# Kernel optimization log

Measured on AMD Instinct MI355X. Metric: run time of the kernel, lower is better.

Reference implementation:

```python
import jax, jax.numpy as jnp
import numpy as np

B, S, E, H = 2, 2048, 1024, 16
DH = E // H  # 64


def setup_inputs() -> dict:
    key = jax.random.key(0)
    ks = jax.random.split(key, 5)
    scale = 1.0 / np.sqrt(E)
    x = jax.random.normal(ks[0], (B, S, E), dtype=jnp.float32)
    # stacked per-head kqv Linear weights: out = x @ Wkqv[h] + bkqv[h], producing (k, q, v) chunks
    Wkqv = jax.random.normal(ks[1], (H, E, 3 * DH), dtype=jnp.float32) * scale
    bkqv = jax.random.normal(ks[2], (H, 3 * DH), dtype=jnp.float32) * scale
    Wo = jax.random.normal(ks[3], (E, E), dtype=jnp.float32) * scale
    bo = jax.random.normal(ks[4], (E,), dtype=jnp.float32) * scale
    return {"x": x, "Wkqv": Wkqv, "bkqv": bkqv, "Wo": Wo, "bo": bo}


def reference(x, Wkqv, bkqv, Wo, bo):
    b, s, e = x.shape
    h, _, f = Wkqv.shape
    dh = f // 3
    # per-head projection, fused over heads: [b, h, s, 3*dh]
    kqv = jnp.einsum('bse,hef->bhsf', x, Wkqv) + bkqv[None, :, None, :]
    # chunk order in the original is k, q, v
    k, q, v = jnp.split(kqv, 3, axis=-1)
    scores = jnp.einsum('bhqd,bhkd->bhqk', q, k) / jnp.sqrt(jnp.asarray(dh, x.dtype))
    causal = jnp.tril(jnp.ones((s, s), dtype=bool))  # slice of the tril buffer
    scores = jnp.where(causal[None, None], scores, -jnp.inf)
    weights = jax.nn.softmax(scores, axis=-1)
    sa = jnp.einsum('bhqk,bhkd->bhqd', weights, v)
    # concat heads along feature dim (head order preserved)
    sa = sa.transpose(0, 2, 1, 3).reshape(b, s, h * dh)
    return sa @ Wo + bo
```

## Files before the change

### kernel.cpp

```cpp
#include <hip/hip_runtime.h>
#include <hip/hip_bf16.h>

typedef __attribute__((ext_vector_type(8))) short bf16x8;
typedef __attribute__((ext_vector_type(4))) float f32x4;
typedef unsigned short u16;

#define NEG_INF (-__builtin_inff())

__device__ __forceinline__ void gload16(const void* g, void* l) {
  __builtin_amdgcn_global_load_lds(
      (const __attribute__((address_space(1))) void*)g,
      (__attribute__((address_space(3))) void*)l, 16, 0, 0);
}

__device__ __forceinline__ u16 f2b(float f) {
  union { float f; unsigned u; } v;
  v.f = f;
  unsigned r = v.u + 0x7fff + ((v.u >> 16) & 1);
  return (u16)(r >> 16);
}

__global__ __launch_bounds__(256) void cvt_f2b_kernel(
    const float* __restrict__ in, u16* __restrict__ out, int n4) {
  int i = blockIdx.x * 256 + threadIdx.x;
  if (i >= n4) return;
  float4 v = ((const float4*)in)[i];
  ushort2 a = {f2b(v.x), f2b(v.y)}, b = {f2b(v.z), f2b(v.w)};
  ((ushort2*)out)[i * 2] = a;
  ((ushort2*)out)[i * 2 + 1] = b;
}

__global__ __launch_bounds__(256) void transpose_f2b(
    const float* __restrict__ src, u16* __restrict__ dst, int R, int C) {
  __shared__ u16 t[32][33];
  int c0 = blockIdx.x * 32, r0 = blockIdx.y * 32;
  const float* s = src + (size_t)blockIdx.z * R * C;
  u16* d = dst + (size_t)blockIdx.z * R * C;
  for (int i = threadIdx.y; i < 32; i += 8)
    t[i][threadIdx.x] = f2b(s[(size_t)(r0 + i) * C + c0 + threadIdx.x]);
  __syncthreads();
  for (int i = threadIdx.y; i < 32; i += 8)
    d[(size_t)(c0 + i) * R + r0 + threadIdx.x] = t[threadIdx.x][i];
}

__device__ __forceinline__ void gemm_mainloop_128(
    const __hip_bfloat16* __restrict__ A, const __hip_bfloat16* __restrict__ Bt,
    int K, int m0, int n0, f32x4 acc[4][4], char* AsB, char* BsB) {
  const int tid = threadIdx.x;
  const int wave = tid >> 6, lane = tid & 63;
  const int lhi = lane >> 4, llo = lane & 15;
  const int wr = wave >> 1, wc = wave & 1;
  f32x4 z = {0.f, 0.f, 0.f, 0.f};
#pragma unroll
  for (int i = 0; i < 4; i++)
#pragma unroll
    for (int j = 0; j < 4; j++) acc[i][j] = z;

#define GSTAGE(c, kk)                                                          \
  {                                                                            \
    char* AsW = AsB + (c)*8192;                                                \
    char* BsW = BsB + (c)*8192;                                                \
    _Pragma("unroll") for (int i = 0; i < 2; i++) {                            \
      int cb = i * 256 + wave * 64;                                            \
      int cq = cb + lane;                                                      \
      gload16(A + ((size_t)(m0 + (cq >> 2)) * K + (kk) + (cq & 3) * 8),        \
              AsW + cb * 16);                                                  \
      gload16(Bt + ((size_t)(n0 + (cq >> 2)) * K + (kk) + (cq & 3) * 8),       \
              BsW + cb * 16);                                                  \
    }                                                                          \
  }

  GSTAGE(0, 0);
  int cur = 0;
  const int nk = K >> 5;
  for (int t = 0; t < nk; t++) {
    if (t + 1 < nk) {
      GSTAGE(cur ^ 1, (t + 1) * 32);
      asm volatile("s_waitcnt vmcnt(4)" ::: "memory");
    } else {
      asm volatile("s_waitcnt vmcnt(0)" ::: "memory");
    }
    __builtin_amdgcn_s_barrier();
    __builtin_amdgcn_sched_barrier(0);

    const char* Ar = AsB + cur * 8192;
    const char* Br = BsB + cur * 8192;
    bf16x8 a[4], b[4];
#pragma unroll
    for (int m4 = 0; m4 < 4; m4++)
      a[m4] = *(const bf16x8*)(Ar + (wr * 64 + m4 * 16 + llo) * 64 + lhi * 16);
#pragma unroll
    for (int n4 = 0; n4 < 4; n4++)
      b[n4] = *(const bf16x8*)(Br + (wc * 64 + n4 * 16 + llo) * 64 + lhi * 16);
#pragma unroll
    for (int m4 = 0; m4 < 4; m4++)
#pragma unroll
      for (int n4 = 0; n4 < 4; n4++)
        acc[m4][n4] =
            __builtin_amdgcn_mfma_f32_16x16x32_bf16(a[m4], b[n4], acc[m4][n4], 0, 0, 0);
    __builtin_amdgcn_sched_barrier(0);
    __builtin_amdgcn_s_barrier();
    cur ^= 1;
  }
#undef GSTAGE
}

__global__ __launch_bounds__(256) void kqv_gemm(
    const __hip_bfloat16* __restrict__ x, const __hip_bfloat16* __restrict__ WT,
    const float* __restrict__ bkqv, __hip_bfloat16* __restrict__ Qb,
    __hip_bfloat16* __restrict__ Kb, __hip_bfloat16* __restrict__ Vt) {
  __shared__ __align__(16) char As[16384];
  __shared__ __align__(16) char Bs[16384];
  const int m0 = blockIdx.y * 128, n0 = blockIdx.x * 128;
  f32x4 acc[4][4];
  gemm_mainloop_128(x, WT, 1024, m0, n0, acc, As, Bs);

  const int tid = threadIdx.x, wave = tid >> 6, lane = tid & 63;
  const int lhi = lane >> 4, llo = lane & 15;
  const int wr = wave >> 1, wc = wave & 1;
#pragma unroll
  for (int m4 = 0; m4 < 4; m4++)
#pragma unroll
    for (int n4 = 0; n4 < 4; n4++)
#pragma unroll
      for (int r = 0; r < 4; r++) {
        int mg = m0 + wr * 64 + m4 * 16 + lhi * 4 + r;
        int ng = n0 + wc * 64 + n4 * 16 + llo;
        int b = mg >> 11, s = mg & 2047;
        int h = ng / 192, f = ng % 192;
        float v = acc[m4][n4][r] + bkqv[h * 192 + f];
        int chunk = f >> 6, d = f & 63;
        size_t bh = (size_t)(b * 16 + h);
        if (chunk == 0)
          Kb[(bh * 2048 + s) * 64 + d] = __float2bfloat16(v);
        else if (chunk == 1)
          Qb[(bh * 2048 + s) * 64 + d] = __float2bfloat16(v * 0.180336880f);
        else
          Vt[(bh * 64 + d) * 2048 + s] = __float2bfloat16(v);
      }
}

__global__ __launch_bounds__(256) void attn_kernel(
    const __hip_bfloat16* __restrict__ Qb, const __hip_bfloat16* __restrict__ Kb,
    const __hip_bfloat16* __restrict__ Vt, __hip_bfloat16* __restrict__ SA) {
  __shared__ __align__(16) char lds[40960];
  const int bx0 = blockIdx.x;
  const int bx = (bx0 & 7) * 64 + (bx0 >> 3);
  const int bh = bx >> 4;
  const int ip = bx & 15;
  const int qa = 31 - ip, qbt = ip;
  const int nta = qa + 1, nt = nta + qbt + 1;
  const int b = bh >> 4, h = bh & 15;
  const int tid = threadIdx.x, wave = tid >> 6, lane = tid & 63;
  const int lhi = lane >> 4, llo = lane & 15;
  const int lhi4 = lhi * 4;

  const __hip_bfloat16* qpA =
      Qb + ((size_t)bh * 2048 + qa * 64 + wave * 16 + llo) * 64 + lhi * 8;
  const __hip_bfloat16* qpB =
      Qb + ((size_t)bh * 2048 + qbt * 64 + wave * 16 + llo) * 64 + lhi * 8;
  bf16x8 qA0 = *(const bf16x8*)qpA, qA1 = *(const bf16x8*)(qpA + 32);
  bf16x8 qB0 = *(const bf16x8*)qpB, qB1 = *(const bf16x8*)(qpB + 32);
  bf16x8 q0 = qA0, q1 = qA1;

  const char* Kg = (const char*)(Kb + (size_t)bh * 2048 * 64);
  const char* Vg = (const char*)(Vt + (size_t)bh * 64 * 2048);
  char* PsB = lds + 32768 + wave * 2048;

  f32x4 z = {0.f, 0.f, 0.f, 0.f};
  f32x4 o[4];
  float m_s = NEG_INF, l_s = 0.f;
#pragma unroll
  for (int i = 0; i < 4; i++) o[i] = z;
  int qg = qa * 64 + wave * 16 + llo;
  int qg0 = qa * 64 + wave * 16 + lhi4;

#define STAGE(c, k0)                                                          \
  {                                                                           \
    char* KsW = lds + (c)*8192;                                               \
    char* VsW = lds + 16384 + (c)*8192;                                       \
    _Pragma("unroll") for (int i = 0; i < 2; i++) {                           \
      int ch = i * 256 + tid;                                                 \
      int soff = (ch * 16) ^ (((ch >> 3) & 7) << 4);                          \
      gload16(Kg + (size_t)(k0)*128 + soff, KsW + (i * 256 + wave * 64) * 16);\
      int dd = ch >> 3, c8 = ch & 7;                                          \
      int boff = (c8 * 16) ^ ((dd & 7) << 4);                                 \
      gload16(Vg + (size_t)dd * 4096 + (size_t)(k0)*2 + boff,                 \
              VsW + (i * 256 + wave * 64) * 16);                              \
    }                                                                         \
  }

  STAGE(0, 0);
  int cur = 0;

  for (int T = 0; T < nt; T++) {
    const int Tn = T + 1;
    if (Tn < nt) {
      const int k0n = (Tn < nta ? Tn : Tn - nta) * 64;
      STAGE(cur ^ 1, k0n);
      asm volatile("s_waitcnt vmcnt(4)" ::: "memory");
    } else {
      asm volatile("s_waitcnt vmcnt(0)" ::: "memory");
    }
    __builtin_amdgcn_s_barrier();
    __builtin_amdgcn_sched_barrier(0);

    const int k0 = (T < nta ? T : T - nta) * 64;
    const bool masked = (T == nta - 1) || (T == nt - 1);
    const char* KsB = lds + cur * 8192;
    const char* VsB = lds + 16384 + cur * 8192;

    f32x4 s[4] = {z, z, z, z};
#pragma unroll
    for (int j = 0; j < 4; j++) {
      const int row = j * 16 + llo;
      const int rx = (row & 7) << 4;
      bf16x8 bk0 = *(const bf16x8*)(KsB + ((row * 128 + lhi * 16) ^ rx));
      bf16x8 bk1 = *(const bf16x8*)(KsB + ((row * 128 + 64 + lhi * 16) ^ rx));
      s[j] = __builtin_amdgcn_mfma_f32_16x16x32_bf16(bk0, q0, s[j], 0, 0, 0);
      s[j] = __builtin_amdgcn_mfma_f32_16x16x32_bf16(bk1, q1, s[j], 0, 0, 0);
    }

    if (masked) {
#pragma unroll
      for (int j = 0; j < 4; j++)
#pragma unroll
        for (int r = 0; r < 4; r++)
          if (k0 + j * 16 + lhi4 + r > qg) s[j][r] = NEG_INF;
    }
    float pmax = s[0][0];
#pragma unroll
    for (int j = 0; j < 4; j++)
#pragma unroll
      for (int r = 0; r < 4; r++) pmax = fmaxf(pmax, s[j][r]);
    pmax = fmaxf(pmax, __shfl_xor(pmax, 16));
    pmax = fmaxf(pmax, __shfl_xor(pmax, 32));
    if (!__all(pmax - m_s <= 5.0f)) {
      const float mn = fmaxf(m_s, pmax);
      const float sc = __builtin_exp2f(m_s - mn);
      m_s = mn;
      l_s *= sc;
#pragma unroll
      for (int r = 0; r < 4; r++) {
        const float scr = __shfl(sc, lhi4 + r);
#pragma unroll
        for (int n4 = 0; n4 < 4; n4++) o[n4][r] *= scr;
      }
    }
    const int px = (llo & 7) << 4;
    float ps = 0.f;
#pragma unroll
    for (int j = 0; j < 4; j++) {
      ushort4 pw;
#pragma unroll
      for (int r = 0; r < 4; r++) {
        const float p = __builtin_exp2f(s[j][r] - m_s);
        ps += p;
        ((__hip_bfloat16*)&pw)[r] = __float2bfloat16(p);
      }
      *(ushort4*)(PsB + ((llo * 128 + j * 32 + lhi * 8) ^ px)) = pw;
    }
    l_s += ps;

    {
      bf16x8 ap0 = *(const bf16x8*)(PsB + ((llo * 128 + lhi * 16) ^ px));
      bf16x8 ap1 = *(const bf16x8*)(PsB + ((llo * 128 + 64 + lhi * 16) ^ px));
#pragma unroll
      for (int n4 = 0; n4 < 4; n4++) {
        const int d = n4 * 16 + llo;
        const int dx = (d & 7) << 4;
        bf16x8 bv0 = *(const bf16x8*)(VsB + ((d * 128 + lhi * 16) ^ dx));
        bf16x8 bv1 = *(const bf16x8*)(VsB + ((d * 128 + 64 + lhi * 16) ^ dx));
        o[n4] = __builtin_amdgcn_mfma_f32_16x16x32_bf16(ap0, bv0, o[n4], 0, 0, 0);
        o[n4] = __builtin_amdgcn_mfma_f32_16x16x32_bf16(ap1, bv1, o[n4], 0, 0, 0);
      }
    }
    __builtin_amdgcn_sched_barrier(0);
    __builtin_amdgcn_s_barrier();

    if (T == nta - 1) {
      float l = l_s;
      l += __shfl_xor(l, 16);
      l += __shfl_xor(l, 32);
      const float inv = 1.f / l;
#pragma unroll
      for (int r = 0; r < 4; r++) {
        const float invr = __shfl(inv, lhi4 + r);
        const size_t ob = ((size_t)b * 2048 + qg0 + r) * 1024 + h * 64;
#pragma unroll
        for (int n4 = 0; n4 < 4; n4++)
          SA[ob + n4 * 16 + llo] = __float2bfloat16(o[n4][r] * invr);
      }
#pragma unroll
      for (int i = 0; i < 4; i++) o[i] = z;
      m_s = NEG_INF;
      l_s = 0.f;
      q0 = qB0; q1 = qB1;
      qg = qbt * 64 + wave * 16 + llo;
      qg0 = qbt * 64 + wave * 16 + lhi4;
    }
    cur ^= 1;
  }

  {
    float l = l_s;
    l += __shfl_xor(l, 16);
    l += __shfl_xor(l, 32);
    const float inv = 1.f / l;
#pragma unroll
    for (int r = 0; r < 4; r++) {
      const float invr = __shfl(inv, lhi4 + r);
      const size_t ob = ((size_t)b * 2048 + qg0 + r) * 1024 + h * 64;
#pragma unroll
      for (int n4 = 0; n4 < 4; n4++)
        SA[ob + n4 * 16 + llo] = __float2bfloat16(o[n4][r] * invr);
    }
  }
#undef STAGE
}

__global__ __launch_bounds__(256) void out_gemm(
    const __hip_bfloat16* __restrict__ SA, const __hip_bfloat16* __restrict__ WoT,
    const float* __restrict__ bo, float* __restrict__ out) {
  __shared__ __align__(16) char As[16384];
  __shared__ __align__(16) char Bs[16384];
  const int m0 = blockIdx.y * 128, n0 = blockIdx.x * 128;
  f32x4 acc[4][4];
  gemm_mainloop_128(SA, WoT, 1024, m0, n0, acc, As, Bs);

  const int tid = threadIdx.x, wave = tid >> 6, lane = tid & 63;
  const int lhi = lane >> 4, llo = lane & 15;
  const int wr = wave >> 1, wc = wave & 1;
#pragma unroll
  for (int m4 = 0; m4 < 4; m4++)
#pragma unroll
    for (int n4 = 0; n4 < 4; n4++)
#pragma unroll
      for (int r = 0; r < 4; r++) {
        int mg = m0 + wr * 64 + m4 * 16 + lhi * 4 + r;
        int ng = n0 + wc * 64 + n4 * 16 + llo;
        out[(size_t)mg * 1024 + ng] = acc[m4][n4][r] + bo[ng];
      }
}

extern "C" void kernel_launch(void* const* d_in, const int* in_sizes, int n_in,
                              void* d_out, int out_size, void* d_ws, size_t ws_size,
                              hipStream_t stream) {
  const float* x = (const float*)d_in[0];
  const float* Wkqv = (const float*)d_in[1];
  const float* bkqv = (const float*)d_in[2];
  const float* Wo = (const float*)d_in[3];
  const float* bo = (const float*)d_in[4];
  float* out = (float*)d_out;

  char* w = (char*)d_ws;
  __hip_bfloat16* WkqvT = (__hip_bfloat16*)(w);
  __hip_bfloat16* WoT = (__hip_bfloat16*)(w + 6291456);
  __hip_bfloat16* Qb = (__hip_bfloat16*)(w + 8388608);
  __hip_bfloat16* Kb = (__hip_bfloat16*)(w + 16777216);
  __hip_bfloat16* Vt = (__hip_bfloat16*)(w + 25165824);
  __hip_bfloat16* SAb = (__hip_bfloat16*)(w + 33554432);
  __hip_bfloat16* xb = (__hip_bfloat16*)(w + 41943040);

  cvt_f2b_kernel<<<4096, 256, 0, stream>>>(x, (u16*)xb, 1048576);
  transpose_f2b<<<dim3(6, 32, 16), dim3(32, 8, 1), 0, stream>>>(
      Wkqv, (u16*)WkqvT, 1024, 192);
  transpose_f2b<<<dim3(32, 32, 1), dim3(32, 8, 1), 0, stream>>>(
      Wo, (u16*)WoT, 1024, 1024);
  kqv_gemm<<<dim3(24, 32), 256, 0, stream>>>(xb, WkqvT, bkqv, Qb, Kb, Vt);
  attn_kernel<<<512, 256, 0, stream>>>(Qb, Kb, Vt, SAb);
  out_gemm<<<dim3(8, 32), 256, 0, stream>>>(SAb, WoT, bo, out);
}
```

Measured before the change: 130.2 us.

## Fuse prep kernels, split attention into one q-tile per block, shrink out GEMM tile

Merges the three conversion/transpose kernels into one prep launch to cut launch overhead. Attention switches from paired heavy/light q-tiles per block to one q-tile per block, launched heaviest first, doubling the grid to 1024 blocks. The output GEMM moves to a 64x128 tile with 512 blocks to fill more CUs. The trade is more blocks with less work each, and tile-level load balance now depends on the hardware scheduler rather than explicit pairing.

```diff
diff --git a/kernel.cpp b/kernel.cpp
--- a/kernel.cpp
+++ b/kernel.cpp
@@ -20,27 +20,42 @@
   return (u16)(r >> 16);
 }
 
-__global__ __launch_bounds__(256) void cvt_f2b_kernel(
-    const float* __restrict__ in, u16* __restrict__ out, int n4) {
-  int i = blockIdx.x * 256 + threadIdx.x;
-  if (i >= n4) return;
-  float4 v = ((const float4*)in)[i];
-  ushort2 a = {f2b(v.x), f2b(v.y)}, b = {f2b(v.z), f2b(v.w)};
-  ((ushort2*)out)[i * 2] = a;
-  ((ushort2*)out)[i * 2 + 1] = b;
-}
-
-__global__ __launch_bounds__(256) void transpose_f2b(
-    const float* __restrict__ src, u16* __restrict__ dst, int R, int C) {
+__global__ __launch_bounds__(256) void prep_kernel(
+    const float* __restrict__ x, u16* __restrict__ xb,
+    const float* __restrict__ Wkqv, u16* __restrict__ WkqvT,
+    const float* __restrict__ Wo, u16* __restrict__ WoT) {
   __shared__ u16 t[32][33];
-  int c0 = blockIdx.x * 32, r0 = blockIdx.y * 32;
-  const float* s = src + (size_t)blockIdx.z * R * C;
-  u16* d = dst + (size_t)blockIdx.z * R * C;
-  for (int i = threadIdx.y; i < 32; i += 8)
-    t[i][threadIdx.x] = f2b(s[(size_t)(r0 + i) * C + c0 + threadIdx.x]);
+  const int bid = blockIdx.x;
+  const int tid = threadIdx.x;
+  if (bid < 4096) {
+    const int i = bid * 256 + tid;
+    float4 v = ((const float4*)x)[i];
+    ushort2 a = {f2b(v.x), f2b(v.y)}, b = {f2b(v.z), f2b(v.w)};
+    ((ushort2*)xb)[i * 2] = a;
+    ((ushort2*)xb)[i * 2 + 1] = b;
+    return;
+  }
+  const int tx = tid & 31, ty = tid >> 5;
+  const float* src;
+  u16* dst;
+  int R, C, bx_, by;
+  if (bid < 7168) {
+    const int tt = bid - 4096;
+    const int bz = tt / 192, rem = tt % 192;
+    by = rem / 6; bx_ = rem % 6; R = 1024; C = 192;
+    src = Wkqv + (size_t)bz * R * C;
+    dst = WkqvT + (size_t)bz * R * C;
+  } else {
+    const int tt = bid - 7168;
+    by = tt >> 5; bx_ = tt & 31; R = 1024; C = 1024;
+    src = Wo; dst = WoT;
+  }
+  const int c0 = bx_ * 32, r0 = by * 32;
+  for (int i = ty; i < 32; i += 8)
+    t[i][tx] = f2b(src[(size_t)(r0 + i) * C + c0 + tx]);
   __syncthreads();
-  for (int i = threadIdx.y; i < 32; i += 8)
-    d[(size_t)(c0 + i) * R + r0 + threadIdx.x] = t[threadIdx.x][i];
+  for (int i = ty; i < 32; i += 8)
+    dst[(size_t)(c0 + i) * R + r0 + tx] = t[tx][i];
 }
 
 __device__ __forceinline__ void gemm_mainloop_128(
@@ -103,6 +118,68 @@
     cur ^= 1;
   }
 #undef GSTAGE
+}
+
+__device__ __forceinline__ void gemm_mainloop_64x128(
+    const __hip_bfloat16* __restrict__ A, const __hip_bfloat16* __restrict__ Bt,
+    int K, int m0, int n0, f32x4 acc[2][4], char* AsB, char* BsB) {
+  const int tid = threadIdx.x;
+  const int wave = tid >> 6, lane = tid & 63;
+  const int lhi = lane >> 4, llo = lane & 15;
+  const int wr = wave >> 1, wc = wave & 1;
+  f32x4 z = {0.f, 0.f, 0.f, 0.f};
+#pragma unroll
+  for (int i = 0; i < 2; i++)
+#pragma unroll
+    for (int j = 0; j < 4; j++) acc[i][j] = z;
+
+#define GSTAGE64(c, kk)                                                        \
+  {                                                                            \
+    char* AsW = AsB + (c)*4096;                                                \
+    char* BsW = BsB + (c)*8192;                                                \
+    gload16(A + ((size_t)(m0 + (tid >> 2)) * K + (kk) + (tid & 3) * 8),        \
+            AsW + (wave * 64) * 16);                                           \
+    _Pragma("unroll") for (int i = 0; i < 2; i++) {                            \
+      int cb = i * 256 + wave * 64;                                            \
+      int cq = cb + lane;                                                      \
+      gload16(Bt + ((size_t)(n0 + (cq >> 2)) * K + (kk) + (cq & 3) * 8),       \
+              BsW + cb * 16);                                                  \
+    }                                                                          \
+  }
+
+  GSTAGE64(0, 0);
+  int cur = 0;
+  const int nk = K >> 5;
+  for (int t = 0; t < nk; t++) {
+    if (t + 1 < nk) {
+      GSTAGE64(cur ^ 1, (t + 1) * 32);
+      asm volatile("s_waitcnt vmcnt(3)" ::: "memory");
+    } else {
+      asm volatile("s_waitcnt vmcnt(0)" ::: "memory");
+    }
+    __builtin_amdgcn_s_barrier();
+    __builtin_amdgcn_sched_barrier(0);
+
+    const char* Ar = AsB + cur * 4096;
+    const char* Br = BsB + cur * 8192;
+    bf16x8 a[2], b[4];
+#pragma unroll
+    for (int m2 = 0; m2 < 2; m2++)
+      a[m2] = *(const bf16x8*)(Ar + (wr * 32 + m2 * 16 + llo) * 64 + lhi * 16);
+#pragma unroll
+    for (int n4 = 0; n4 < 4; n4++)
+      b[n4] = *(const bf16x8*)(Br + (wc * 64 + n4 * 16 + llo) * 64 + lhi * 16);
+#pragma unroll
+    for (int m2 = 0; m2 < 2; m2++)
+#pragma unroll
+      for (int n4 = 0; n4 < 4; n4++)
+        acc[m2][n4] =
+            __builtin_amdgcn_mfma_f32_16x16x32_bf16(a[m2], b[n4], acc[m2][n4], 0, 0, 0);
+    __builtin_amdgcn_sched_barrier(0);
+    __builtin_amdgcn_s_barrier();
+    cur ^= 1;
+  }
+#undef GSTAGE64
 }
 
 __global__ __launch_bounds__(256) void kqv_gemm(
@@ -144,24 +221,18 @@
     const __hip_bfloat16* __restrict__ Qb, const __hip_bfloat16* __restrict__ Kb,
     const __hip_bfloat16* __restrict__ Vt, __hip_bfloat16* __restrict__ SA) {
   __shared__ __align__(16) char lds[40960];
-  const int bx0 = blockIdx.x;
-  const int bx = (bx0 & 7) * 64 + (bx0 >> 3);
-  const int bh = bx >> 4;
-  const int ip = bx & 15;
-  const int qa = 31 - ip, qbt = ip;
-  const int nta = qa + 1, nt = nta + qbt + 1;
+  const int orig = blockIdx.x;
+  const int bh = (orig & 7) * 4 + ((orig >> 3) & 3);
+  const int qt = 31 - (orig >> 5);
+  const int nt = qt + 1;
   const int b = bh >> 4, h = bh & 15;
   const int tid = threadIdx.x, wave = tid >> 6, lane = tid & 63;
   const int lhi = lane >> 4, llo = lane & 15;
   const int lhi4 = lhi * 4;
 
-  const __hip_bfloat16* qpA =
-      Qb + ((size_t)bh * 2048 + qa * 64 + wave * 16 + llo) * 64 + lhi * 8;
-  const __hip_bfloat16* qpB =
-      Qb + ((size_t)bh * 2048 + qbt * 64 + wave * 16 + llo) * 64 + lhi * 8;
-  bf16x8 qA0 = *(const bf16x8*)qpA, qA1 = *(const bf16x8*)(qpA + 32);
-  bf16x8 qB0 = *(const bf16x8*)qpB, qB1 = *(const bf16x8*)(qpB + 32);
-  bf16x8 q0 = qA0, q1 = qA1;
+  const __hip_bfloat16* qp =
+      Qb + ((size_t)bh * 2048 + qt * 64 + wave * 16 + llo) * 64 + lhi * 8;
+  bf16x8 q0 = *(const bf16x8*)qp, q1 = *(const bf16x8*)(qp + 32);
 
   const char* Kg = (const char*)(Kb + (size_t)bh * 2048 * 64);
   const char* Vg = (const char*)(Vt + (size_t)bh * 64 * 2048);
@@ -172,8 +243,8 @@
   float m_s = NEG_INF, l_s = 0.f;
 #pragma unroll
   for (int i = 0; i < 4; i++) o[i] = z;
-  int qg = qa * 64 + wave * 16 + llo;
-  int qg0 = qa * 64 + wave * 16 + lhi4;
+  const int qg = qt * 64 + wave * 16 + llo;
+  const int qg0 = qt * 64 + wave * 16 + lhi4;
 
 #define STAGE(c, k0)                                                          \
   {                                                                           \
@@ -194,10 +265,8 @@
   int cur = 0;
 
   for (int T = 0; T < nt; T++) {
-    const int Tn = T + 1;
-    if (Tn < nt) {
-      const int k0n = (Tn < nta ? Tn : Tn - nta) * 64;
-      STAGE(cur ^ 1, k0n);
+    if (T + 1 < nt) {
+      STAGE(cur ^ 1, (T + 1) * 64);
       asm volatile("s_waitcnt vmcnt(4)" ::: "memory");
     } else {
       asm volatile("s_waitcnt vmcnt(0)" ::: "memory");
@@ -205,8 +274,8 @@
     __builtin_amdgcn_s_barrier();
     __builtin_amdgcn_sched_barrier(0);
 
-    const int k0 = (T < nta ? T : T - nta) * 64;
-    const bool masked = (T == nta - 1) || (T == nt - 1);
+    const int k0 = T * 64;
+    const bool masked = (T == nt - 1);
     const char* KsB = lds + cur * 8192;
     const char* VsB = lds + 16384 + cur * 8192;
 
@@ -277,28 +346,6 @@
     }
     __builtin_amdgcn_sched_barrier(0);
     __builtin_amdgcn_s_barrier();
-
-    if (T == nta - 1) {
-      float l = l_s;
-      l += __shfl_xor(l, 16);
-      l += __shfl_xor(l, 32);
-      const float inv = 1.f / l;
-#pragma unroll
-      for (int r = 0; r < 4; r++) {
-        const float invr = __shfl(inv, lhi4 + r);
-        const size_t ob = ((size_t)b * 2048 + qg0 + r) * 1024 + h * 64;
-#pragma unroll
-        for (int n4 = 0; n4 < 4; n4++)
-          SA[ob + n4 * 16 + llo] = __float2bfloat16(o[n4][r] * invr);
-      }
-#pragma unroll
-      for (int i = 0; i < 4; i++) o[i] = z;
-      m_s = NEG_INF;
-      l_s = 0.f;
-      q0 = qB0; q1 = qB1;
-      qg = qbt * 64 + wave * 16 + llo;
-      qg0 = qbt * 64 + wave * 16 + lhi4;
-    }
     cur ^= 1;
   }
 
@@ -322,24 +369,24 @@
 __global__ __launch_bounds__(256) void out_gemm(
     const __hip_bfloat16* __restrict__ SA, const __hip_bfloat16* __restrict__ WoT,
     const float* __restrict__ bo, float* __restrict__ out) {
-  __shared__ __align__(16) char As[16384];
+  __shared__ __align__(16) char As[8192];
   __shared__ __align__(16) char Bs[16384];
-  const int m0 = blockIdx.y * 128, n0 = blockIdx.x * 128;
-  f32x4 acc[4][4];
-  gemm_mainloop_128(SA, WoT, 1024, m0, n0, acc, As, Bs);
+  const int m0 = blockIdx.y * 64, n0 = blockIdx.x * 128;
+  f32x4 acc[2][4];
+  gemm_mainloop_64x128(SA, WoT, 1024, m0, n0, acc, As, Bs);
 
   const int tid = threadIdx.x, wave = tid >> 6, lane = tid & 63;
   const int lhi = lane >> 4, llo = lane & 15;
   const int wr = wave >> 1, wc = wave & 1;
 #pragma unroll
-  for (int m4 = 0; m4 < 4; m4++)
+  for (int m2 = 0; m2 < 2; m2++)
 #pragma unroll
     for (int n4 = 0; n4 < 4; n4++)
 #pragma unroll
       for (int r = 0; r < 4; r++) {
-        int mg = m0 + wr * 64 + m4 * 16 + lhi * 4 + r;
+        int mg = m0 + wr * 32 + m2 * 16 + lhi * 4 + r;
         int ng = n0 + wc * 64 + n4 * 16 + llo;
-        out[(size_t)mg * 1024 + ng] = acc[m4][n4][r] + bo[ng];
+        out[(size_t)mg * 1024 + ng] = acc[m2][n4][r] + bo[ng];
       }
 }
 
@@ -362,12 +409,9 @@
   __hip_bfloat16* SAb = (__hip_bfloat16*)(w + 33554432);
   __hip_bfloat16* xb = (__hip_bfloat16*)(w + 41943040);
 
-  cvt_f2b_kernel<<<4096, 256, 0, stream>>>(x, (u16*)xb, 1048576);
-  transpose_f2b<<<dim3(6, 32, 16), dim3(32, 8, 1), 0, stream>>>(
-      Wkqv, (u16*)WkqvT, 1024, 192);
-  transpose_f2b<<<dim3(32, 32, 1), dim3(32, 8, 1), 0, stream>>>(
-      Wo, (u16*)WoT, 1024, 1024);
+  prep_kernel<<<8192, 256, 0, stream>>>(x, (u16*)xb, Wkqv, (u16*)WkqvT,
+                                        Wo, (u16*)WoT);
   kqv_gemm<<<dim3(24, 32), 256, 0, stream>>>(xb, WkqvT, bkqv, Qb, Kb, Vt);
-  attn_kernel<<<512, 256, 0, stream>>>(Qb, Kb, Vt, SAb);
-  out_gemm<<<dim3(8, 32), 256, 0, stream>>>(SAb, WoT, bo, out);
-}
+  attn_kernel<<<1024, 256, 0, stream>>>(Qb, Kb, Vt, SAb);
+  out_gemm<<<dim3(8, 64), 256, 0, stream>>>(SAb, WoT, bo, out);
+}
```

New measurement: 117.2 us. 1.11x faster.
